# Performance work log

Measured on AMD Instinct MI355X. Metric: run time of the kernel, lower is better.

The kernel has to match this reference:

```python
import jax
import jax.numpy as jnp
from jax import lax
import numpy as np

SLIDING_WINDOW_LEN = 192
EPS = 1e-6


def setup_inputs() -> dict:
    key = jax.random.key(0)
    X = jax.random.normal(key, (8, 8, 257, 2000), dtype=jnp.float32)
    return {"X": X, "ref_channel": 0}


def _forgetting_normalization(XrMag):
    # XrMag: [B, 1, F, T] magnitude of reference channel
    alpha = (SLIDING_WINDOW_LEN - 1) / (SLIDING_WINDOW_LEN + 1)
    # mean over frequency, keepdim -> [B, 1, 1, T]
    XrMM = XrMag.mean(axis=2, keepdims=True)
    T = XrMM.shape[-1]
    t = jnp.arange(T, dtype=XrMM.dtype)
    # original: alpha_this = min((t-1)/(t+1), alpha) for t < L, else alpha;
    # since (t-1)/(t+1) >= alpha for t >= L, a single minimum is exact.
    a = jnp.minimum((t - 1.0) / (t + 1.0), alpha)  # [T]

    x_seq = jnp.moveaxis(XrMM, -1, 0)  # [T, B, 1, 1]
    mu0 = jnp.zeros_like(x_seq[0])

    def step(mu, inp):
        a_t, x_t = inp
        mu = a_t * mu + (1.0 - a_t) * x_t
        return mu, mu

    _, mus = lax.scan(step, mu0, (a, x_seq))  # [T, B, 1, 1]
    return jnp.moveaxis(mus, 0, -1)  # [B, 1, 1, T]


def reference(X, ref_channel):
    # X: [B, C, F, T] (real stand-in for complex); ref_channel: python int
    Xr = X[:, ref_channel:ref_channel + 1]  # [B, 1, F, T]
    XrMag = jnp.abs(Xr)
    # original detaches XrMM (.detach().cpu()) -> stop_gradient
    XrMM = lax.stop_gradient(_forgetting_normalization(XrMag)) + EPS  # [B,1,1,T]
    X_norm = X / XrMM  # broadcast over C, F
    return X_norm
```

## Files before the change

### kernel.cpp

```cpp
#include <hip/hip_runtime.h>

#define B_N 8
#define C_N 8
#define F_N 257
#define T_N 2000
#define EPSF 1e-6f

#define FCH 16
#define FPC 17

__global__ __launch_bounds__(512) void partial_mean_kernel(
    const float* __restrict__ X, const int* __restrict__ ref_ch,
    float4* __restrict__ part4 )
{
    const int b   = blockIdx.x;
    const int c   = blockIdx.y;
    const int tid = threadIdx.x;
    if (tid >= T_N / 4) return;

    const int rc = ref_ch[0];
    const float4* Xb4 =
        (const float4*)(X + ((size_t)(b * C_N + rc)) * (size_t)F_N * T_N);

    const int f0 = c * FPC;
    const int f1 = (f0 + FPC < F_N) ? (f0 + FPC) : F_N;

    float ax = 0.f, ay = 0.f, az = 0.f, aw = 0.f;
    for (int f = f0; f < f1; ++f) {
        float4 v = Xb4[f * (T_N / 4) + tid];
        ax += fabsf(v.x); ay += fabsf(v.y);
        az += fabsf(v.z); aw += fabsf(v.w);
    }
    part4[(b * FCH + c) * (T_N / 4) + tid] = make_float4(ax, ay, az, aw);
}

__global__ __launch_bounds__(512) void scan_kernel(
    const float4* __restrict__ part4,
    float4* __restrict__ inv4 )
{
    __shared__ float s_mean[T_N];
    __shared__ float s_wA[8];
    __shared__ float s_wB[8];
    const float ALPHA = (float)(191.0 / 193.0);

    const int b   = blockIdx.x;
    const int tid = threadIdx.x;

    if (tid < T_N / 4) {
        float ax = 0.f, ay = 0.f, az = 0.f, aw = 0.f;
        #pragma unroll
        for (int c = 0; c < FCH; ++c) {
            float4 v = part4[(b * FCH + c) * (T_N / 4) + tid];
            ax += v.x; ay += v.y; az += v.z; aw += v.w;
        }
        const int t = tid * 4;
        const float inv_f = 1.f / (float)F_N;
        s_mean[t + 0] = ax * inv_f;
        s_mean[t + 1] = ay * inv_f;
        s_mean[t + 2] = az * inv_f;
        s_mean[t + 3] = aw * inv_f;
    }
    __syncthreads();

    float A = 1.f, Bv = 0.f;
    const int tbase = tid * 4;
    #pragma unroll
    for (int k = 0; k < 4; ++k) {
        const int t = tbase + k;
        if (t < T_N) {
            const float tf = (float)t;
            const float a = fminf((tf - 1.f) / (tf + 1.f), ALPHA);
            const float x = s_mean[t];
            Bv = a * Bv + (1.f - a) * x;
            A  = a * A;
        }
    }

    const int lane = tid & 63;
    #pragma unroll
    for (int d = 1; d < 64; d <<= 1) {
        const float pA = __shfl_up(A, d);
        const float pB = __shfl_up(Bv, d);
        if (lane >= d) {
            Bv = A * pB + Bv;
            A  = A * pA;
        }
    }

    const int wid = tid >> 6;
    if (lane == 63) { s_wA[wid] = A; s_wB[wid] = Bv; }
    __syncthreads();
    if (tid == 0) {
        float cA = 1.f, cB = 0.f;
        #pragma unroll
        for (int w = 0; w < 8; ++w) {
            const float nA = s_wA[w] * cA;
            const float nB = s_wA[w] * cB + s_wB[w];
            s_wA[w] = cA; s_wB[w] = cB;
            cA = nA; cB = nB;
        }
    }
    __syncthreads();

    float eA = __shfl_up(A, 1);
    float eB = __shfl_up(Bv, 1);
    if (lane == 0) { eA = 1.f; eB = 0.f; }
    float mu = eA * s_wB[wid] + eB;

    if (tid < T_N / 4) {
        float r[4];
        #pragma unroll
        for (int k = 0; k < 4; ++k) {
            const int t = tbase + k;
            const float tf = (float)t;
            const float a = fminf((tf - 1.f) / (tf + 1.f), ALPHA);
            const float x = s_mean[t];
            mu = a * mu + (1.f - a) * x;
            r[k] = 1.f / (mu + EPSF);
        }
        inv4[b * (T_N / 4) + tid] = make_float4(r[0], r[1], r[2], r[3]);
    }
}

__global__ __launch_bounds__(256) void norm_kernel(
    const float4* __restrict__ X4,
    const float4* __restrict__ inv4,
    float4* __restrict__ out4)
{
    const int N4    = B_N * C_N * F_N * T_N / 4;
    const int PER_B = C_N * F_N * T_N / 4;
    const int idx = blockIdx.x * 256 + threadIdx.x;
    if (idx >= N4) return;

    const int b  = idx / PER_B;
    const int tq = idx % (T_N / 4);

    const float4 iv = inv4[b * (T_N / 4) + tq];
    const float4 x  = X4[idx];
    out4[idx] = make_float4(x.x * iv.x, x.y * iv.y, x.z * iv.z, x.w * iv.w);
}

extern "C" void kernel_launch(void* const* d_in, const int* in_sizes, int n_in,
                              void* d_out, int out_size, void* d_ws, size_t ws_size,
                              hipStream_t stream) {
    const float* X  = (const float*)d_in[0];
    const int*   rc = (const int*)d_in[1];

    float* inv  = (float*)d_ws;
    float* part = (float*)d_ws + B_N * T_N;

    dim3 gA(B_N, FCH);
    partial_mean_kernel<<<gA, 512, 0, stream>>>(X, rc, (float4*)part);

    scan_kernel<<<B_N, 512, 0, stream>>>((const float4*)part, (float4*)inv);

    const int N4 = B_N * C_N * F_N * T_N / 4;
    norm_kernel<<<(N4 + 255) / 256, 256, 0, stream>>>(
        (const float4*)X, (const float4*)inv, (float4*)d_out);
}
```

Before: 55.51 us.

## Use nontemporal vector loads/stores, 2D norm grid, and finer partial-mean split

The normalization kernel now uses nontemporal loads and stores on native vector types, and its grid is 2D with the batch taken from blockIdx.y, which removes a large integer division per thread. The partial-mean stage splits frequency into 32 chunks instead of 16 to launch more blocks. The scan then reads more partial sums, and nontemporal hints may not help if the cache policy was already fine.

New measurement: 56.86 us (median of 4 runs). 2.4% more time.

```diff
diff --git a/kernel.cpp b/kernel.cpp
--- a/kernel.cpp
+++ b/kernel.cpp
@@ -6,12 +6,14 @@
 #define T_N 2000
 #define EPSF 1e-6f
 
-#define FCH 16
-#define FPC 17
+#define FCH 32
+#define FPC 9
+
+typedef float f32x4 __attribute__((ext_vector_type(4)));
 
 __global__ __launch_bounds__(512) void partial_mean_kernel(
     const float* __restrict__ X, const int* __restrict__ ref_ch,
-    float4* __restrict__ part4 )
+    f32x4* __restrict__ part4 )
 {
     const int b   = blockIdx.x;
     const int c   = blockIdx.y;
@@ -19,24 +21,24 @@
     if (tid >= T_N / 4) return;
 
     const int rc = ref_ch[0];
-    const float4* Xb4 =
-        (const float4*)(X + ((size_t)(b * C_N + rc)) * (size_t)F_N * T_N);
+    const f32x4* Xb4 =
+        (const f32x4*)(X + ((size_t)(b * C_N + rc)) * (size_t)F_N * T_N);
 
     const int f0 = c * FPC;
     const int f1 = (f0 + FPC < F_N) ? (f0 + FPC) : F_N;
 
-    float ax = 0.f, ay = 0.f, az = 0.f, aw = 0.f;
+    f32x4 acc = {0.f, 0.f, 0.f, 0.f};
     for (int f = f0; f < f1; ++f) {
-        float4 v = Xb4[f * (T_N / 4) + tid];
-        ax += fabsf(v.x); ay += fabsf(v.y);
-        az += fabsf(v.z); aw += fabsf(v.w);
+        f32x4 v = Xb4[f * (T_N / 4) + tid];
+        acc.x += fabsf(v.x); acc.y += fabsf(v.y);
+        acc.z += fabsf(v.z); acc.w += fabsf(v.w);
     }
-    part4[(b * FCH + c) * (T_N / 4) + tid] = make_float4(ax, ay, az, aw);
+    part4[(b * FCH + c) * (T_N / 4) + tid] = acc;
 }
 
 __global__ __launch_bounds__(512) void scan_kernel(
-    const float4* __restrict__ part4,
-    float4* __restrict__ inv4 )
+    const f32x4* __restrict__ part4,
+    f32x4* __restrict__ inv4 )
 {
     __shared__ float s_mean[T_N];
     __shared__ float s_wA[8];
@@ -47,18 +49,16 @@
     const int tid = threadIdx.x;
 
     if (tid < T_N / 4) {
-        float ax = 0.f, ay = 0.f, az = 0.f, aw = 0.f;
+        f32x4 s = {0.f, 0.f, 0.f, 0.f};
         #pragma unroll
-        for (int c = 0; c < FCH; ++c) {
-            float4 v = part4[(b * FCH + c) * (T_N / 4) + tid];
-            ax += v.x; ay += v.y; az += v.z; aw += v.w;
-        }
+        for (int c = 0; c < FCH; ++c)
+            s += part4[(b * FCH + c) * (T_N / 4) + tid];
         const int t = tid * 4;
         const float inv_f = 1.f / (float)F_N;
-        s_mean[t + 0] = ax * inv_f;
-        s_mean[t + 1] = ay * inv_f;
-        s_mean[t + 2] = az * inv_f;
-        s_mean[t + 3] = aw * inv_f;
+        s_mean[t + 0] = s.x * inv_f;
+        s_mean[t + 1] = s.y * inv_f;
+        s_mean[t + 2] = s.z * inv_f;
+        s_mean[t + 3] = s.w * inv_f;
     }
     __syncthreads();
 
@@ -108,7 +108,7 @@
     float mu = eA * s_wB[wid] + eB;
 
     if (tid < T_N / 4) {
-        float r[4];
+        f32x4 r;
         #pragma unroll
         for (int k = 0; k < 4; ++k) {
             const int t = tbase + k;
@@ -118,26 +118,25 @@
             mu = a * mu + (1.f - a) * x;
             r[k] = 1.f / (mu + EPSF);
         }
-        inv4[b * (T_N / 4) + tid] = make_float4(r[0], r[1], r[2], r[3]);
+        inv4[b * (T_N / 4) + tid] = r;
     }
 }
 
 __global__ __launch_bounds__(256) void norm_kernel(
-    const float4* __restrict__ X4,
-    const float4* __restrict__ inv4,
-    float4* __restrict__ out4)
+    const f32x4* __restrict__ X4,
+    const f32x4* __restrict__ inv4,
+    f32x4* __restrict__ out4)
 {
-    const int N4    = B_N * C_N * F_N * T_N / 4;
     const int PER_B = C_N * F_N * T_N / 4;
-    const int idx = blockIdx.x * 256 + threadIdx.x;
-    if (idx >= N4) return;
+    const int i  = blockIdx.x * 256 + threadIdx.x;
+    if (i >= PER_B) return;
+    const int b  = blockIdx.y;
+    const int tq = i % (T_N / 4);
 
-    const int b  = idx / PER_B;
-    const int tq = idx % (T_N / 4);
-
-    const float4 iv = inv4[b * (T_N / 4) + tq];
-    const float4 x  = X4[idx];
-    out4[idx] = make_float4(x.x * iv.x, x.y * iv.y, x.z * iv.z, x.w * iv.w);
+    const size_t g = (size_t)b * PER_B + i;
+    const f32x4 iv = inv4[b * (T_N / 4) + tq];
+    const f32x4 x  = __builtin_nontemporal_load(X4 + g);
+    __builtin_nontemporal_store(x * iv, out4 + g);
 }
 
 extern "C" void kernel_launch(void* const* d_in, const int* in_sizes, int n_in,
@@ -150,11 +149,12 @@
     float* part = (float*)d_ws + B_N * T_N;
 
     dim3 gA(B_N, FCH);
-    partial_mean_kernel<<<gA, 512, 0, stream>>>(X, rc, (float4*)part);
+    partial_mean_kernel<<<gA, 512, 0, stream>>>(X, rc, (f32x4*)part);
 
-    scan_kernel<<<B_N, 512, 0, stream>>>((const float4*)part, (float4*)inv);
+    scan_kernel<<<B_N, 512, 0, stream>>>((const f32x4*)part, (f32x4*)inv);
 
-    const int N4 = B_N * C_N * F_N * T_N / 4;
-    norm_kernel<<<(N4 + 255) / 256, 256, 0, stream>>>(
-        (const float4*)X, (const float4*)inv, (float4*)d_out);
+    const int PER_B = C_N * F_N * T_N / 4;
+    dim3 gC((PER_B + 255) / 256, B_N);
+    norm_kernel<<<gC, 256, 0, stream>>>(
+        (const f32x4*)X, (const f32x4*)inv, (f32x4*)d_out);
 }
```
